# Performance work log

Measured on AMD Instinct MI355X. Metric: run time of the kernel, lower is better.

Reference implementation:

```python
import jax, jax.numpy as jnp
import numpy as np

B, LA, LB = 16, 2048, 2048
DA, DB, DH = 768, 512, 512
EPS = 1e-5


def _layer_norm(x, g, b):
    mu = jnp.mean(x, axis=-1, keepdims=True)
    var = jnp.var(x, axis=-1, keepdims=True)
    return (x - mu) * jax.lax.rsqrt(var + EPS) * g + b


def setup_inputs() -> dict:
    key = jax.random.key(0)
    ks = jax.random.split(key, 12)
    s = lambda d: 1.0 / np.sqrt(d)
    return {
        "z_a": jax.random.normal(ks[0], (B, LA, DA), jnp.float32),
        "z_b": jax.random.normal(ks[1], (B, LB, DB), jnp.float32),
        "Wa": jax.random.uniform(ks[2], (DA, DH), jnp.float32, -s(DA), s(DA)),
        "ba": jnp.zeros((DH,), jnp.float32),
        "Wb": jax.random.uniform(ks[3], (DB, DH), jnp.float32, -s(DB), s(DB)),
        "bb": jnp.zeros((DH,), jnp.float32),
        "W_co": jax.random.normal(ks[4], (DH, DH), jnp.float32),
        "Woa": jax.random.uniform(ks[5], (DH, DA), jnp.float32, -s(DH), s(DH)),
        "boa": jnp.zeros((DA,), jnp.float32),
        "Wob": jax.random.uniform(ks[6], (DH, DB), jnp.float32, -s(DH), s(DH)),
        "bob": jnp.zeros((DB,), jnp.float32),
        "ga": jnp.ones((DA,), jnp.float32),
        "beta_a": jnp.zeros((DA,), jnp.float32),
        "gb": jnp.ones((DB,), jnp.float32),
        "beta_b": jnp.zeros((DB,), jnp.float32),
    }


def reference(z_a, z_b, Wa, ba, Wb, bb, W_co, Woa, boa, Wob, bob, ga, beta_a, gb, beta_b):
    # projections to shared hidden space
    h_a = jnp.einsum('bld,dh->blh', z_a, Wa) + ba          # (B, LA, DH)
    h_b = jnp.einsum('bld,dh->blh', z_b, Wb) + bb          # (B, LB, DH)
    # bilinear tanh co-attention scores
    C = jnp.tanh(jnp.einsum('bih,hk,bjk->bij', h_a, W_co, h_b))  # (B, LA, LB)
    attn_a = jax.nn.softmax(C, axis=-1)                    # rows: over LB
    attn_b = jax.nn.softmax(C.transpose(0, 2, 1), axis=-1) # cols: over LA
    h_a_co = jnp.einsum('bij,bjh->bih', attn_a, h_b)       # (B, LA, DH)
    h_b_co = jnp.einsum('bji,bih->bjh', attn_b, h_a)       # (B, LB, DH)
    z_a_co = jnp.einsum('blh,hd->bld', h_a_co, Woa) + boa
    z_b_co = jnp.einsum('blh,hd->bld', h_b_co, Wob) + bob
    z_a_out = _layer_norm(z_a + z_a_co, ga, beta_a)
    z_b_out = _layer_norm(z_b + z_b_co, gb, beta_b)
    return (z_a_out, z_b_out)
```

## Files before the change

kernel.cpp:

```cpp
#include <hip/hip_runtime.h>
#include <stdint.h>

typedef short bf16x8 __attribute__((ext_vector_type(8)));
typedef float f32x16 __attribute__((ext_vector_type(16)));

#define BM 256
#define BN 256
#define BK 64
#define ABUF_U 16384
#define BUF_U  32768

#define AS1 __attribute__((address_space(1)))
#define AS3 __attribute__((address_space(3)))

__device__ __forceinline__ ushort f2bf(float x) {
    uint32_t u = __float_as_uint(x);
    u += 0x7FFFu + ((u >> 16) & 1u);
    return (ushort)(u >> 16);
}
__device__ __forceinline__ float bf2f(ushort u) {
    return __uint_as_float((uint)u << 16);
}

__device__ __forceinline__ void gload16(const void* g, void* l) {
    __builtin_amdgcn_global_load_lds((const AS1 void*)g, (AS3 void*)l, 16, 0, 0);
}

#define ISSUE2(kt, buf, i0)                                                          \
    do {                                                                             \
        gload16(((i0) < 4 ? Ap : Bp) + goff[i0] + (kt), smem + (buf)*BUF_U + loff[i0]); \
        gload16((((i0)+1) < 4 ? Ap : Bp) + goff[(i0)+1] + (kt), smem + (buf)*BUF_U + loff[(i0)+1]); \
    } while (0)

template<int MODE, bool HAS_BIAS, bool WRITE_T>
__global__ __launch_bounds__(512, 2)
void gemm_bt(const ushort* __restrict__ Aptr_, const ushort* __restrict__ Bptr_,
             void* __restrict__ Cptr_, ushort* __restrict__ CTptr_,
             const float* __restrict__ bias, const ushort* __restrict__ resid_,
             float* __restrict__ rsum_, float* __restrict__ csum_,
             const float* __restrict__ scale_,
             int M, int N, int K, int lda, int ldb, int ldc,
             long sA, long sB, long sC, long sCT, long sSum,
             int ldct, int rbshift)
{
    extern __shared__ ushort smem[];

    const int gx = gridDim.x, gy = gridDim.y;
    const int nwg = gx * gy * (int)gridDim.z;
    int flat = ((int)blockIdx.z * gy + (int)blockIdx.y) * gx + (int)blockIdx.x;
    {
        const int q8 = nwg >> 3, r8 = nwg & 7;
        const int xcd = flat & 7, loc = flat >> 3;
        flat = (xcd < r8 ? xcd * (q8 + 1) : r8 * (q8 + 1) + (xcd - r8) * q8) + loc;
    }
    const int z   = flat / (gx * gy);
    const int rem = flat - z * (gx * gy);
    const int m0  = (rem % gx) * BM;
    const int n0  = (rem / gx) * BN;

    const int tid  = threadIdx.x;
    const int lane = tid & 63;
    const int wave = tid >> 6;
    const int wr   = wave >> 2;
    const int wcn  = wave & 3;
    const int lr   = lane & 31, lh = lane >> 5;

    const ushort* Ap = Aptr_ + z * sA;
    const ushort* Bp = Bptr_ + z * sB;

    long goff[8]; int loff[8];
    #pragma unroll
    for (int u = 0; u < 4; ++u) {
        const int li  = u * 512 + tid;
        const int row = li >> 3;
        const int gck = (li & 7) ^ (row & 7);
        goff[u]     = (long)(m0 + row) * lda + gck * 8;
        loff[u]     = li * 8;
        goff[u + 4] = (long)(n0 + row) * ldb + gck * 8;
        loff[u + 4] = ABUF_U + li * 8;
    }

    f32x16 acc[4][2] = {};

    const int nk = K / BK;
    ISSUE2(0, 0, 0); ISSUE2(0, 0, 2); ISSUE2(0, 0, 4); ISSUE2(0, 0, 6);

    for (int t = 0; t < nk; ++t) {
        const int cur = t & 1, nxt = cur ^ 1;
        const ushort* As = smem + cur * BUF_U;
        const ushort* Bs = As + ABUF_U;
        const bool pf = (t + 1 < nk);
        const int kt1 = (t + 1) * BK;

        if (pf) {
            ISSUE2(kt1, nxt, 0);
            asm volatile("s_waitcnt vmcnt(2)" ::: "memory");
        } else {
            asm volatile("s_waitcnt vmcnt(0)" ::: "memory");
        }
        __builtin_amdgcn_s_barrier();

        #pragma unroll
        for (int kk = 0; kk < 4; ++kk) {
            bf16x8 af[4], bfv[2];
            #pragma unroll
            for (int tm = 0; tm < 4; ++tm) {
                const int row = wr * 128 + tm * 32 + lr;
                const int ck  = (kk * 2 + lh) ^ (row & 7);
                af[tm] = *(const bf16x8*)&As[row * BK + ck * 8];
            }
            #pragma unroll
            for (int tn = 0; tn < 2; ++tn) {
                const int row = wcn * 64 + tn * 32 + lr;
                const int ck  = (kk * 2 + lh) ^ (row & 7);
                bfv[tn] = *(const bf16x8*)&Bs[row * BK + ck * 8];
            }
            if (pf) {
                if (kk == 0)      ISSUE2(kt1, nxt, 2);
                else if (kk == 1) ISSUE2(kt1, nxt, 4);
                else if (kk == 2) ISSUE2(kt1, nxt, 6);
            }
            #pragma unroll
            for (int tm = 0; tm < 4; ++tm)
                #pragma unroll
                for (int tn = 0; tn < 2; ++tn)
                    acc[tm][tn] = __builtin_amdgcn_mfma_f32_32x32x16_bf16(
                        af[tm], bfv[tn], acc[tm][tn], 0, 0, 0);
        }

        asm volatile("s_waitcnt lgkmcnt(0)" ::: "memory");
        __builtin_amdgcn_s_barrier();
    }

    const int colb0 = n0 + wcn * 64 + lr;
    const int rowbw = m0 + wr * 128 + 4 * lh;

    if constexpr (MODE == 3) {
        ushort* Cp = (ushort*)Cptr_;
        #pragma unroll
        for (int tm = 0; tm < 4; ++tm)
            #pragma unroll
            for (int tn = 0; tn < 2; ++tn) {
                const int col = colb0 + tn * 32;
                const float bv = bias[col];
                #pragma unroll
                for (int q = 0; q < 4; ++q)
                    #pragma unroll
                    for (int s = 0; s < 4; ++s) {
                        const int row = rowbw + tm * 32 + q * 8 + s;
                        const long idx = (long)row * ldc + col;
                        Cp[idx] = f2bf(acc[tm][tn][q * 4 + s] + bv + bf2f(resid_[idx]));
                    }
            }
    } else if constexpr (MODE == 0) {
        ushort* Cp = (ushort*)Cptr_ + z * sC;
        #pragma unroll
        for (int tm = 0; tm < 4; ++tm)
            #pragma unroll
            for (int tn = 0; tn < 2; ++tn) {
                const int col = colb0 + tn * 32;
                const float bv = HAS_BIAS ? bias[col] : 0.f;
                ushort us[16];
                #pragma unroll
                for (int rr = 0; rr < 16; ++rr) us[rr] = f2bf(acc[tm][tn][rr] + bv);
                #pragma unroll
                for (int q = 0; q < 4; ++q)
                    #pragma unroll
                    for (int s = 0; s < 4; ++s)
                        Cp[(long)(rowbw + tm * 32 + q * 8 + s) * ldc + col] = us[q * 4 + s];
                if constexpr (WRITE_T) {
                    #pragma unroll
                    for (int q = 0; q < 4; ++q) {
                        const int gr = rowbw + tm * 32 + q * 8;
                        const int bb = gr >> rbshift;
                        const int ii = gr & ((1 << rbshift) - 1);
                        *(ushort4*)&CTptr_[(long)bb * sCT + (long)col * ldct + ii] =
                            make_ushort4(us[q * 4 + 0], us[q * 4 + 1], us[q * 4 + 2], us[q * 4 + 3]);
                    }
                }
            }
    } else if constexpr (MODE == 1) {
        ushort* Ep  = (ushort*)Cptr_ + z * sC;
        ushort* ETp = CTptr_ + z * sCT;
        float* rs = rsum_ + z * sSum;
        float* cs = csum_ + z * sSum;
        float colp[2] = {0.f, 0.f};
        #pragma unroll
        for (int tm = 0; tm < 4; ++tm) {
            float rowp[16];
            #pragma unroll
            for (int rr = 0; rr < 16; ++rr) rowp[rr] = 0.f;
            #pragma unroll
            for (int tn = 0; tn < 2; ++tn) {
                const int col = colb0 + tn * 32;
                ushort us[16];
                #pragma unroll
                for (int rr = 0; rr < 16; ++rr) {
                    const float x  = acc[tm][tn][rr];
                    const float th = 1.f - 2.f / (__expf(2.f * x) + 1.f);
                    const float e  = __expf(th);
                    rowp[rr] += e;
                    colp[tn] += e;
                    us[rr] = f2bf(e);
                }
                #pragma unroll
                for (int q = 0; q < 4; ++q) {
                    #pragma unroll
                    for (int s = 0; s < 4; ++s)
                        Ep[(long)(rowbw + tm * 32 + q * 8 + s) * ldc + col] = us[q * 4 + s];
                    const int gr = rowbw + tm * 32 + q * 8;
                    *(ushort4*)&ETp[(long)col * ldct + gr] =
                        make_ushort4(us[q * 4 + 0], us[q * 4 + 1], us[q * 4 + 2], us[q * 4 + 3]);
                }
            }
            #pragma unroll
            for (int rr = 0; rr < 16; ++rr) {
                float v = rowp[rr];
                v += __shfl_xor(v, 1);  v += __shfl_xor(v, 2);
                v += __shfl_xor(v, 4);  v += __shfl_xor(v, 8);
                v += __shfl_xor(v, 16);
                if (lr == 0)
                    atomicAdd(&rs[rowbw + tm * 32 + (rr & 3) + 8 * (rr >> 2)], v);
            }
        }
        #pragma unroll
        for (int tn = 0; tn < 2; ++tn) {
            float v = colp[tn];
            v += __shfl_xor(v, 32);
            if (lh == 0) atomicAdd(&cs[colb0 + tn * 32], v);
        }
    } else {
        const float* sc = scale_ + z * sSum;
        ushort* Cp = (ushort*)Cptr_ + z * sC;
        #pragma unroll
        for (int tm = 0; tm < 4; ++tm) {
            float rcp[16];
            #pragma unroll
            for (int rr = 0; rr < 16; ++rr)
                rcp[rr] = 1.f / sc[rowbw + tm * 32 + (rr & 3) + 8 * (rr >> 2)];
            #pragma unroll
            for (int tn = 0; tn < 2; ++tn) {
                const int col = colb0 + tn * 32;
                #pragma unroll
                for (int q = 0; q < 4; ++q)
                    #pragma unroll
                    for (int s = 0; s < 4; ++s)
                        Cp[(long)(rowbw + tm * 32 + q * 8 + s) * ldc + col] =
                            f2bf(acc[tm][tn][q * 4 + s] * rcp[q * 4 + s]);
            }
        }
    }
}

__global__ __launch_bounds__(256)
void cast32to16(const float* __restrict__ in, ushort* __restrict__ out, long n) {
    const long stride = (long)gridDim.x * 256 * 8;
    for (long i = ((long)blockIdx.x * 256 + threadIdx.x) * 8; i < n; i += stride) {
        const float4 f0 = *(const float4*)(in + i);
        const float4 f1 = *(const float4*)(in + i + 4);
        uint4 w;
        w.x = (uint)f2bf(f0.x) | ((uint)f2bf(f0.y) << 16);
        w.y = (uint)f2bf(f0.z) | ((uint)f2bf(f0.w) << 16);
        w.z = (uint)f2bf(f1.x) | ((uint)f2bf(f1.y) << 16);
        w.w = (uint)f2bf(f1.z) | ((uint)f2bf(f1.w) << 16);
        *(uint4*)(out + i) = w;
    }
}

__global__ __launch_bounds__(256)
void tcast(const float* __restrict__ in, ushort* __restrict__ out, int R, int C) {
    __shared__ float t[32][33];
    const int bx = blockIdx.x * 32, by = blockIdx.y * 32;
    const int tx = threadIdx.x, ty = threadIdx.y;
    for (int i = ty; i < 32; i += 8) {
        const int r = by + i, cc = bx + tx;
        if (r < R && cc < C) t[i][tx] = in[(long)r * C + cc];
    }
    __syncthreads();
    for (int i = ty; i < 32; i += 8) {
        const int cc = bx + i, r = by + tx;
        if (cc < C && r < R) out[(long)cc * R + r] = f2bf(t[tx][i]);
    }
}

template<int D>
__global__ __launch_bounds__(D / 4)
void ln_bf(const ushort* __restrict__ y, float* __restrict__ out,
           const float* __restrict__ gam, const float* __restrict__ bet) {
    constexpr int NW = D / 256;
    const long row = blockIdx.x;
    const int tid = threadIdx.x;
    const ushort4 v4 = *(const ushort4*)&y[row * D + tid * 4];
    float v[4] = {bf2f(v4.x), bf2f(v4.y), bf2f(v4.z), bf2f(v4.w)};
    float s = v[0] + v[1] + v[2] + v[3];
    float s2 = v[0]*v[0] + v[1]*v[1] + v[2]*v[2] + v[3]*v[3];
    #pragma unroll
    for (int off = 1; off < 64; off <<= 1) {
        s  += __shfl_xor(s, off);
        s2 += __shfl_xor(s2, off);
    }
    __shared__ float ws[4], ws2[4];
    const int wave = tid >> 6, lane = tid & 63;
    if (lane == 0) { ws[wave] = s; ws2[wave] = s2; }
    __syncthreads();
    s = 0.f; s2 = 0.f;
    #pragma unroll
    for (int w2 = 0; w2 < NW; ++w2) { s += ws[w2]; s2 += ws2[w2]; }
    const float mu   = s / D;
    const float var  = s2 / D - mu * mu;
    const float rstd = rsqrtf(var + 1e-5f);
    const float4 gv = *(const float4*)&gam[tid * 4];
    const float4 bv = *(const float4*)&bet[tid * 4];
    float4 o;
    o.x = (v[0] - mu) * rstd * gv.x + bv.x;
    o.y = (v[1] - mu) * rstd * gv.y + bv.y;
    o.z = (v[2] - mu) * rstd * gv.z + bv.z;
    o.w = (v[3] - mu) * rstd * gv.w + bv.w;
    *(float4*)&out[row * D + tid * 4] = o;
}

extern "C" void kernel_launch(void* const* d_in, const int* in_sizes, int n_in,
                              void* d_out, int out_size, void* d_ws, size_t ws_size,
                              hipStream_t stream)
{
    (void)in_sizes; (void)n_in; (void)out_size; (void)ws_size;
    const float* z_a    = (const float*)d_in[0];
    const float* z_b    = (const float*)d_in[1];
    const float* Wa     = (const float*)d_in[2];
    const float* ba     = (const float*)d_in[3];
    const float* Wb     = (const float*)d_in[4];
    const float* bb     = (const float*)d_in[5];
    const float* Wco    = (const float*)d_in[6];
    const float* Woa    = (const float*)d_in[7];
    const float* boa    = (const float*)d_in[8];
    const float* Wob    = (const float*)d_in[9];
    const float* bob    = (const float*)d_in[10];
    const float* ga     = (const float*)d_in[11];
    const float* beta_a = (const float*)d_in[12];
    const float* gb     = (const float*)d_in[13];
    const float* beta_b = (const float*)d_in[14];

    const int Bn = 16, LA = 2048, LB = 2048, DA = 768, DB = 512, DH = 512;
    const long MA = (long)Bn * LA;
    const long MB = (long)Bn * LB;

    char* w = (char*)d_ws;
    size_t off = 0;
    auto alc = [&](size_t bytes) { void* p = w + off; off += (bytes + 255) & ~(size_t)255; return p; };

    ushort* WaT  = (ushort*)alc((size_t)DH * DA * 2);
    ushort* WbT  = (ushort*)alc((size_t)DH * DB * 2);
    ushort* WcoT = (ushort*)alc((size_t)DH * DH * 2);
    ushort* WoaT = (ushort*)alc((size_t)DA * DH * 2);
    ushort* WobT = (ushort*)alc((size_t)DB * DH * 2);
    ushort* h_a  = (ushort*)alc((size_t)MA * DH * 2);
    ushort* h_b  = (ushort*)alc((size_t)MB * DH * 2);
    ushort* h_aT = (ushort*)alc((size_t)Bn * DH * LA * 2);
    ushort* h_bT = (ushort*)alc((size_t)Bn * DH * LB * 2);
    ushort* Ma   = (ushort*)alc((size_t)MA * DH * 2);
    ushort* E    = (ushort*)alc((size_t)Bn * LA * LB * 2);
    ushort* ET   = (ushort*)alc((size_t)Bn * LB * LA * 2);
    ushort* Pa   = (ushort*)alc((size_t)MA * DH * 2);
    ushort* Pb   = (ushort*)alc((size_t)MB * DH * 2);
    float*  rsum = (float*)alc((size_t)Bn * LA * 4);
    float*  csum = (float*)alc((size_t)Bn * LB * 4);

    ushort* za16 = (ushort*)d_out;
    ushort* zb16 = za16 + (size_t)MA * DA;
    ushort* yA = E;
    ushort* yB = E + (size_t)MA * DA;

    dim3 blk(512, 1, 1);
    dim3 blk256(256, 1, 1);
    dim3 tb(32, 8, 1);
    const int SHM = 2 * BUF_U * 2;

    tcast<<<dim3(DH / 32, DA / 32, 1), tb, 0, stream>>>(Wa,  WaT,  DA, DH);
    tcast<<<dim3(DH / 32, DB / 32, 1), tb, 0, stream>>>(Wb,  WbT,  DB, DH);
    tcast<<<dim3(DH / 32, DH / 32, 1), tb, 0, stream>>>(Wco, WcoT, DH, DH);
    tcast<<<dim3(DA / 32, DH / 32, 1), tb, 0, stream>>>(Woa, WoaT, DH, DA);
    tcast<<<dim3(DB / 32, DH / 32, 1), tb, 0, stream>>>(Wob, WobT, DH, DB);

    cast32to16<<<dim3(2048, 1, 1), blk256, 0, stream>>>(z_a, za16, MA * DA);
    cast32to16<<<dim3(2048, 1, 1), blk256, 0, stream>>>(z_b, zb16, MB * DB);

    hipMemsetAsync(rsum, 0, (size_t)Bn * (LA + LB) * sizeof(float), stream);

    gemm_bt<0, true, true><<<dim3(MA / BM, DH / BN, 1), blk, SHM, stream>>>(
        za16, WaT, h_a, h_aT, ba, nullptr, nullptr, nullptr, nullptr,
        (int)MA, DH, DA, DA, DA, DH, 0, 0, 0, (long)DH * LA, 0, LA, 11);

    gemm_bt<0, true, true><<<dim3(MB / BM, DH / BN, 1), blk, SHM, stream>>>(
        zb16, WbT, h_b, h_bT, bb, nullptr, nullptr, nullptr, nullptr,
        (int)MB, DH, DB, DB, DB, DH, 0, 0, 0, (long)DH * LB, 0, LB, 11);

    gemm_bt<0, false, false><<<dim3(MA / BM, DH / BN, 1), blk, SHM, stream>>>(
        h_a, WcoT, Ma, nullptr, nullptr, nullptr, nullptr, nullptr, nullptr,
        (int)MA, DH, DH, DH, DH, DH, 0, 0, 0, 0, 0, 0, 0);

    gemm_bt<1, false, false><<<dim3(LA / BM, LB / BN, Bn), blk, SHM, stream>>>(
        Ma, h_b, E, ET, nullptr, nullptr, rsum, csum, nullptr,
        LA, LB, DH, DH, DH, LB,
        (long)LA * DH, (long)LB * DH, (long)LA * LB, (long)LB * LA, LA, LA, 0);

    gemm_bt<2, false, false><<<dim3(LA / BM, DH / BN, Bn), blk, SHM, stream>>>(
        E, h_bT, Pa, nullptr, nullptr, nullptr, nullptr, nullptr, rsum,
        LA, DH, LB, LB, LB, DH,
        (long)LA * LB, (long)DH * LB, (long)LA * DH, 0, LA, 0, 0);

    gemm_bt<2, false, false><<<dim3(LB / BM, DH / BN, Bn), blk, SHM, stream>>>(
        ET, h_aT, Pb, nullptr, nullptr, nullptr, nullptr, nullptr, csum,
        LB, DH, LA, LA, LA, DH,
        (long)LB * LA, (long)DH * LA, (long)LB * DH, 0, LB, 0, 0);

    gemm_bt<3, true, false><<<dim3(MA / BM, DA / BN, 1), blk, SHM, stream>>>(
        Pa, WoaT, yA, nullptr, boa, za16, nullptr, nullptr, nullptr,
        (int)MA, DA, DH, DH, DH, DA, 0, 0, 0, 0, 0, 0, 0);

    gemm_bt<3, true, false><<<dim3(MB / BM, DB / BN, 1), blk, SHM, stream>>>(
        Pb, WobT, yB, nullptr, bob, zb16, nullptr, nullptr, nullptr,
        (int)MB, DB, DH, DH, DH, DB, 0, 0, 0, 0, 0, 0, 0);

    float* outA = (float*)d_out;
    float* outB = outA + MA * DA;
    ln_bf<768><<<dim3((unsigned)MA, 1, 1), dim3(192, 1, 1), 0, stream>>>(yA, outA, ga, beta_a);
    ln_bf<512><<<dim3((unsigned)MB, 1, 1), dim3(128, 1, 1), 0, stream>>>(yB, outB, gb, beta_b);
}
```

Baseline: 662.2 us.

## Chunk score matrices over batch halves and merge both PV GEMMs into one launch

The score/exp GEMM and the two attention-weighted GEMMs now run in two chunks of 8 batches each. The E and ET buffers shrink to half size and are reused, so each chunk's score matrices (8×2048×2048 bf16, about 64MB each) may stay resident in the large last-level cache between the write and the read-back. The two PV GEMMs (E·h_b and ET·h_a) are fused into a single launch that picks its pointers by z index, which doubles the grid and removes one launch per chunk. This costs more launches for the score stage and less parallelism per score launch. yB is moved into ET to keep the buffer aliasing valid after the shrink.

Measured after the change: 654.3 us. No clear change (-1.2%).

```diff
diff --git a/kernel.cpp b/kernel.cpp
--- a/kernel.cpp
+++ b/kernel.cpp
@@ -39,6 +39,8 @@
              const float* __restrict__ bias, const ushort* __restrict__ resid_,
              float* __restrict__ rsum_, float* __restrict__ csum_,
              const float* __restrict__ scale_,
+             const ushort* __restrict__ Aptr2_, const ushort* __restrict__ Bptr2_,
+             void* __restrict__ Cptr2_, const float* __restrict__ scale2_, int zsplit,
              int M, int N, int K, int lda, int ldb, int ldc,
              long sA, long sB, long sC, long sCT, long sSum,
              int ldct, int rbshift)
@@ -58,6 +60,9 @@
     const int m0  = (rem % gx) * BM;
     const int n0  = (rem / gx) * BN;
 
+    const bool sec = (z >= zsplit);
+    const int  zl  = sec ? z - zsplit : z;
+
     const int tid  = threadIdx.x;
     const int lane = tid & 63;
     const int wave = tid >> 6;
@@ -65,8 +70,8 @@
     const int wcn  = wave & 3;
     const int lr   = lane & 31, lh = lane >> 5;
 
-    const ushort* Ap = Aptr_ + z * sA;
-    const ushort* Bp = Bptr_ + z * sB;
+    const ushort* Ap = (sec ? Aptr2_ : Aptr_) + (long)zl * sA;
+    const ushort* Bp = (sec ? Bptr2_ : Bptr_) + (long)zl * sB;
 
     long goff[8]; int loff[8];
     #pragma unroll
@@ -153,7 +158,7 @@
                     }
             }
     } else if constexpr (MODE == 0) {
-        ushort* Cp = (ushort*)Cptr_ + z * sC;
+        ushort* Cp = (ushort*)Cptr_ + zl * sC;
         #pragma unroll
         for (int tm = 0; tm < 4; ++tm)
             #pragma unroll
@@ -180,10 +185,10 @@
                 }
             }
     } else if constexpr (MODE == 1) {
-        ushort* Ep  = (ushort*)Cptr_ + z * sC;
-        ushort* ETp = CTptr_ + z * sCT;
-        float* rs = rsum_ + z * sSum;
-        float* cs = csum_ + z * sSum;
+        ushort* Ep  = (ushort*)Cptr_ + zl * sC;
+        ushort* ETp = CTptr_ + zl * sCT;
+        float* rs = rsum_ + zl * sSum;
+        float* cs = csum_ + zl * sSum;
         float colp[2] = {0.f, 0.f};
         #pragma unroll
         for (int tm = 0; tm < 4; ++tm) {
@@ -230,8 +235,8 @@
             if (lh == 0) atomicAdd(&cs[colb0 + tn * 32], v);
         }
     } else {
-        const float* sc = scale_ + z * sSum;
-        ushort* Cp = (ushort*)Cptr_ + z * sC;
+        const float* sc = (sec ? scale2_ : scale_) + zl * sSum;
+        ushort* Cp = (ushort*)(sec ? Cptr2_ : Cptr_) + zl * sC;
         #pragma unroll
         for (int tm = 0; tm < 4; ++tm) {
             float rcp[16];
@@ -341,6 +346,7 @@
     const float* beta_b = (const float*)d_in[14];
 
     const int Bn = 16, LA = 2048, LB = 2048, DA = 768, DB = 512, DH = 512;
+    const int ZC = 8;
     const long MA = (long)Bn * LA;
     const long MB = (long)Bn * LB;
 
@@ -358,8 +364,8 @@
     ushort* h_aT = (ushort*)alc((size_t)Bn * DH * LA * 2);
     ushort* h_bT = (ushort*)alc((size_t)Bn * DH * LB * 2);
     ushort* Ma   = (ushort*)alc((size_t)MA * DH * 2);
-    ushort* E    = (ushort*)alc((size_t)Bn * LA * LB * 2);
-    ushort* ET   = (ushort*)alc((size_t)Bn * LB * LA * 2);
+    ushort* E    = (ushort*)alc((size_t)ZC * LA * LB * 2);
+    ushort* ET   = (ushort*)alc((size_t)ZC * LB * LA * 2);
     ushort* Pa   = (ushort*)alc((size_t)MA * DH * 2);
     ushort* Pb   = (ushort*)alc((size_t)MB * DH * 2);
     float*  rsum = (float*)alc((size_t)Bn * LA * 4);
@@ -368,12 +374,13 @@
     ushort* za16 = (ushort*)d_out;
     ushort* zb16 = za16 + (size_t)MA * DA;
     ushort* yA = E;
-    ushort* yB = E + (size_t)MA * DA;
+    ushort* yB = ET;
 
     dim3 blk(512, 1, 1);
     dim3 blk256(256, 1, 1);
     dim3 tb(32, 8, 1);
     const int SHM = 2 * BUF_U * 2;
+    const int NOSPLIT = 1 << 30;
 
     tcast<<<dim3(DH / 32, DA / 32, 1), tb, 0, stream>>>(Wa,  WaT,  DA, DH);
     tcast<<<dim3(DH / 32, DB / 32, 1), tb, 0, stream>>>(Wb,  WbT,  DB, DH);
@@ -388,37 +395,50 @@
 
     gemm_bt<0, true, true><<<dim3(MA / BM, DH / BN, 1), blk, SHM, stream>>>(
         za16, WaT, h_a, h_aT, ba, nullptr, nullptr, nullptr, nullptr,
+        nullptr, nullptr, nullptr, nullptr, NOSPLIT,
         (int)MA, DH, DA, DA, DA, DH, 0, 0, 0, (long)DH * LA, 0, LA, 11);
 
     gemm_bt<0, true, true><<<dim3(MB / BM, DH / BN, 1), blk, SHM, stream>>>(
         zb16, WbT, h_b, h_bT, bb, nullptr, nullptr, nullptr, nullptr,
+        nullptr, nullptr, nullptr, nullptr, NOSPLIT,
         (int)MB, DH, DB, DB, DB, DH, 0, 0, 0, (long)DH * LB, 0, LB, 11);
 
     gemm_bt<0, false, false><<<dim3(MA / BM, DH / BN, 1), blk, SHM, stream>>>(
         h_a, WcoT, Ma, nullptr, nullptr, nullptr, nullptr, nullptr, nullptr,
+        nullptr, nullptr, nullptr, nullptr, NOSPLIT,
         (int)MA, DH, DH, DH, DH, DH, 0, 0, 0, 0, 0, 0, 0);
 
-    gemm_bt<1, false, false><<<dim3(LA / BM, LB / BN, Bn), blk, SHM, stream>>>(
-        Ma, h_b, E, ET, nullptr, nullptr, rsum, csum, nullptr,
-        LA, LB, DH, DH, DH, LB,
-        (long)LA * DH, (long)LB * DH, (long)LA * LB, (long)LB * LA, LA, LA, 0);
-
-    gemm_bt<2, false, false><<<dim3(LA / BM, DH / BN, Bn), blk, SHM, stream>>>(
-        E, h_bT, Pa, nullptr, nullptr, nullptr, nullptr, nullptr, rsum,
-        LA, DH, LB, LB, LB, DH,
-        (long)LA * LB, (long)DH * LB, (long)LA * DH, 0, LA, 0, 0);
-
-    gemm_bt<2, false, false><<<dim3(LB / BM, DH / BN, Bn), blk, SHM, stream>>>(
-        ET, h_aT, Pb, nullptr, nullptr, nullptr, nullptr, nullptr, csum,
-        LB, DH, LA, LA, LA, DH,
-        (long)LB * LA, (long)DH * LA, (long)LB * DH, 0, LB, 0, 0);
+    for (int c = 0; c < Bn / ZC; ++c) {
+        const ushort* Ma_c  = Ma   + (size_t)c * ZC * LA * DH;
+        const ushort* hb_c  = h_b  + (size_t)c * ZC * LB * DH;
+        const ushort* hbT_c = h_bT + (size_t)c * ZC * DH * LB;
+        const ushort* haT_c = h_aT + (size_t)c * ZC * DH * LA;
+        ushort* Pa_c = Pa + (size_t)c * ZC * LA * DH;
+        ushort* Pb_c = Pb + (size_t)c * ZC * LB * DH;
+        float* rs_c = rsum + (size_t)c * ZC * LA;
+        float* cs_c = csum + (size_t)c * ZC * LB;
+
+        gemm_bt<1, false, false><<<dim3(LA / BM, LB / BN, ZC), blk, SHM, stream>>>(
+            Ma_c, hb_c, E, ET, nullptr, nullptr, rs_c, cs_c, nullptr,
+            nullptr, nullptr, nullptr, nullptr, NOSPLIT,
+            LA, LB, DH, DH, DH, LB,
+            (long)LA * DH, (long)LB * DH, (long)LA * LB, (long)LB * LA, LA, LA, 0);
+
+        gemm_bt<2, false, false><<<dim3(LA / BM, DH / BN, 2 * ZC), blk, SHM, stream>>>(
+            E, hbT_c, Pa_c, nullptr, nullptr, nullptr, nullptr, nullptr, rs_c,
+            ET, haT_c, Pb_c, cs_c, ZC,
+            LA, DH, LB, LB, LB, DH,
+            (long)LA * LB, (long)DH * LB, (long)LA * DH, 0, LA, 0, 0);
+    }
 
     gemm_bt<3, true, false><<<dim3(MA / BM, DA / BN, 1), blk, SHM, stream>>>(
         Pa, WoaT, yA, nullptr, boa, za16, nullptr, nullptr, nullptr,
+        nullptr, nullptr, nullptr, nullptr, NOSPLIT,
         (int)MA, DA, DH, DH, DH, DA, 0, 0, 0, 0, 0, 0, 0);
 
     gemm_bt<3, true, false><<<dim3(MB / BM, DB / BN, 1), blk, SHM, stream>>>(
         Pb, WobT, yB, nullptr, bob, zb16, nullptr, nullptr, nullptr,
+        nullptr, nullptr, nullptr, nullptr, NOSPLIT,
         (int)MB, DB, DH, DH, DH, DB, 0, 0, 0, 0, 0, 0, 0);
 
     float* outA = (float*)d_out;
```
